# Kernel tuning notes

Measured on AMD Instinct MI355X. Metric: run time of the kernel, lower is better.

## Reference

```python
import jax, jax.numpy as jnp
import numpy as np

B, N, D_NODE, D_PAIR, D_HID = 1, 384, 256, 128, 32
EPS = 1e-5


def setup_inputs() -> dict:
    key = jax.random.key(0)
    ks = jax.random.split(key, 9)
    sc = lambda fan_in: 1.0 / np.sqrt(fan_in)
    return {
        "s": jax.random.normal(ks[0], (B, N, D_NODE), dtype=jnp.float32),
        "gamma": jnp.ones((D_NODE,), dtype=jnp.float32),
        "beta": jnp.zeros((D_NODE,), dtype=jnp.float32),
        "Wa": jax.random.uniform(ks[1], (D_HID, D_NODE), jnp.float32, -sc(D_NODE), sc(D_NODE)),
        "ba": jax.random.uniform(ks[2], (D_HID,), jnp.float32, -sc(D_NODE), sc(D_NODE)),
        "Wb": jax.random.uniform(ks[3], (D_HID, D_NODE), jnp.float32, -sc(D_NODE), sc(D_NODE)),
        "bb": jax.random.uniform(ks[4], (D_HID,), jnp.float32, -sc(D_NODE), sc(D_NODE)),
        "Wo": jax.random.uniform(ks[5], (D_PAIR, D_HID * D_HID), jnp.float32, -sc(D_HID * D_HID), sc(D_HID * D_HID)),
        "bo": jax.random.uniform(ks[6], (D_PAIR,), jnp.float32, -sc(D_HID * D_HID), sc(D_HID * D_HID)),
    }


def reference(s, gamma, beta, Wa, ba, Wb, bb, Wo, bo):
    # LayerNorm over d_node
    mu = jnp.mean(s, axis=-1, keepdims=True)
    var = jnp.mean(jnp.square(s - mu), axis=-1, keepdims=True)
    sn = (s - mu) * jax.lax.rsqrt(var + EPS) * gamma + beta
    # Projections to d_hidden
    a = jnp.einsum('bnd,hd->bnh', sn, Wa) + ba  # [B,N,H]
    b = jnp.einsum('bnd,hd->bnh', sn, Wb) + bb  # [B,N,H]
    # outer[b,i,j,d,e] = a[b,i,d]*b[b,j,e]; reshape flattens (d,e) with d major,
    # matching Wo.reshape(d_pair, H, H). Fuse the outer product with the output
    # projection to avoid materializing the [B,N,N,H,H] tensor.
    Wr = Wo.reshape(D_PAIR, D_HID, D_HID)
    out = jnp.einsum('bid,bje,pde->bijp', a, b, Wr) + bo  # [B,N,N,d_pair]
    return out
```

## Files before the change

### kernel.cpp

```cpp
#include <hip/hip_runtime.h>
#include <hip/hip_bf16.h>

#define NTOK   384
#define DNODE  256
#define DPAIR  128
#define DHID   32
#define NOUT   49152
static constexpr float LN_EPS = 1e-5f;

typedef __bf16 bf16x8 __attribute__((ext_vector_type(8)));
typedef float  f32x4  __attribute__((ext_vector_type(4)));

__global__ __launch_bounds__(256) void k1_ln_proj(
    const float* __restrict__ s, const float* __restrict__ gamma,
    const float* __restrict__ beta,
    const float* __restrict__ Wa, const float* __restrict__ ba,
    const float* __restrict__ Wb, const float* __restrict__ bb,
    const float* __restrict__ Wo,
    __bf16* __restrict__ a_vec, __bf16* __restrict__ b_vec,
    __bf16* __restrict__ wo_bf)
{
    const int t = threadIdx.x;
    const int blk = blockIdx.x;

    if (blk >= NTOK) {
        const int base = (blk - NTOK) * 1024 + t;
        #pragma unroll
        for (int i = 0; i < 4; ++i)
            wo_bf[base + i * 256] = (__bf16)Wo[base + i * 256];
        return;
    }

    __shared__ __align__(16) float sn[DNODE];
    __shared__ float red[8];

    const float x = s[blk * DNODE + t];
    float v0 = x, v1 = x * x;
    #pragma unroll
    for (int off = 32; off > 0; off >>= 1) {
        v0 += __shfl_down(v0, off, 64);
        v1 += __shfl_down(v1, off, 64);
    }
    if ((t & 63) == 0) { red[(t >> 6) * 2] = v0; red[(t >> 6) * 2 + 1] = v1; }
    __syncthreads();
    const float sum   = red[0] + red[2] + red[4] + red[6];
    const float sumsq = red[1] + red[3] + red[5] + red[7];
    const float mu  = sum * (1.0f / DNODE);
    const float var = sumsq * (1.0f / DNODE) - mu * mu;
    const float inv = rsqrtf(var + LN_EPS);
    sn[t] = (x - mu) * inv * gamma[t] + beta[t];
    __syncthreads();

    const int o = t >> 2, part = t & 3;
    const float* Wrow = (o < DHID) ? (Wa + (size_t)o * DNODE)
                                   : (Wb + (size_t)(o - DHID) * DNODE);
    const int base = part * 64;
    float acc = 0.f;
    #pragma unroll
    for (int k = 0; k < 64; k += 4) {
        const float4 w  = *(const float4*)(Wrow + base + k);
        const float4 xs = *(const float4*)(sn + base + k);
        acc += w.x * xs.x + w.y * xs.y + w.z * xs.z + w.w * xs.w;
    }
    acc += __shfl_xor(acc, 1, 64);
    acc += __shfl_xor(acc, 2, 64);
    if (part == 0) {
        if (o < DHID) a_vec[blk * DHID + o]          = (__bf16)(acc + ba[o]);
        else          b_vec[blk * DHID + (o - DHID)] = (__bf16)(acc + bb[o - DHID]);
    }
}

__global__ __launch_bounds__(256) void k2_build_T(
    const __bf16* __restrict__ b_vec, const __bf16* __restrict__ wo_bf,
    __bf16* __restrict__ Tm)
{
    const int l = threadIdx.x & 63;
    const int w = threadIdx.x >> 6;
    const int j0 = blockIdx.y * 16;
    const int n0 = (blockIdx.x * 4 + w) * 16;
    const int row = l & 15, q = l >> 4, koff = q * 8;

    const bf16x8 af = *(const bf16x8*)(b_vec + (j0 + row) * DHID + koff);
    const bf16x8 bf = *(const bf16x8*)(wo_bf + (size_t)(n0 + row) * 32 + koff);
    f32x4 acc = {0.f, 0.f, 0.f, 0.f};
    acc = __builtin_amdgcn_mfma_f32_16x16x32_bf16(af, bf, acc, 0, 0, 0);

    const int col = n0 + row;
    #pragma unroll
    for (int r = 0; r < 4; ++r)
        Tm[(size_t)(j0 + q * 4 + r) * 4096 + col] = (__bf16)acc[r];
}

__global__ __launch_bounds__(256) void k3_main(
    const __bf16* __restrict__ a_vec, const __bf16* __restrict__ Tm,
    const float* __restrict__ bo, float* __restrict__ out)
{
    const int l = threadIdx.x & 63;
    const int w = threadIdx.x >> 6;
    const int i0 = blockIdx.y * 16;
    const int row = l & 15, q = l >> 4, koff = q * 8;

    const bf16x8 af = *(const bf16x8*)(a_vec + (i0 + row) * DHID + koff);

    const int ntb = blockIdx.x * 16 + w * 4;
    #pragma unroll
    for (int tt = 0; tt < 4; ++tt) {
        const int n0 = (ntb + tt) * 16;
        const bf16x8 bf = *(const bf16x8*)(Tm + (size_t)(n0 + row) * 32 + koff);
        const float bv = bo[(n0 + row) & (DPAIR - 1)];
        f32x4 acc = {bv, bv, bv, bv};
        acc = __builtin_amdgcn_mfma_f32_16x16x32_bf16(af, bf, acc, 0, 0, 0);

        const size_t colbase = (size_t)n0 + row;
        #pragma unroll
        for (int r = 0; r < 4; ++r)
            __builtin_nontemporal_store(
                acc[r], out + (size_t)(i0 + q * 4 + r) * NOUT + colbase);
    }
}

extern "C" void kernel_launch(void* const* d_in, const int* in_sizes, int n_in,
                              void* d_out, int out_size, void* d_ws, size_t ws_size,
                              hipStream_t stream)
{
    const float* s     = (const float*)d_in[0];
    const float* gamma = (const float*)d_in[1];
    const float* beta  = (const float*)d_in[2];
    const float* Wa    = (const float*)d_in[3];
    const float* ba    = (const float*)d_in[4];
    const float* Wb    = (const float*)d_in[5];
    const float* bb    = (const float*)d_in[6];
    const float* Wo    = (const float*)d_in[7];
    const float* bo    = (const float*)d_in[8];
    float* out = (float*)d_out;

    char* ws = (char*)d_ws;
    __bf16* a_vec = (__bf16*)(ws);
    __bf16* b_vec = (__bf16*)(ws + 24576);
    __bf16* wo_bf = (__bf16*)(ws + 49152);
    __bf16* Tm    = (__bf16*)(ws + 311296);

    k1_ln_proj<<<512, 256, 0, stream>>>(s, gamma, beta, Wa, ba, Wb, bb, Wo,
                                        a_vec, b_vec, wo_bf);
    k2_build_T<<<dim3(64, 24), 256, 0, stream>>>(b_vec, wo_bf, Tm);
    k3_main<<<dim3(192, 24), 256, 0, stream>>>(a_vec, Tm, bo, out);
}
```

Baseline: 116.6 us.

## Swap MFMA operand roles for vectorized stores and fold Wo bf16 cast into T build

Drops the separate Wo-to-bf16 conversion pass and instead converts Wo inline inside k2, where it is now the A operand. Both k2 and k3 swap MFMA operand roles so each lane holds four consecutive output columns. This lets them use vectorized bf16x4 and float4 nontemporal stores in place of scattered scalar stores. k3 also handles eight tiles per wave with fewer blocks, and the bias is loaded as a float4. The aim is better store coalescing on the large output write and less launch and workspace traffic, at the cost of redoing the fp32-to-bf16 Wo conversion for every j block.

```diff
diff --git a/kernel.cpp b/kernel.cpp
--- a/kernel.cpp
+++ b/kernel.cpp
@@ -9,6 +9,7 @@
 static constexpr float LN_EPS = 1e-5f;
 
 typedef __bf16 bf16x8 __attribute__((ext_vector_type(8)));
+typedef __bf16 bf16x4 __attribute__((ext_vector_type(4)));
 typedef float  f32x4  __attribute__((ext_vector_type(4)));
 
 __global__ __launch_bounds__(256) void k1_ln_proj(
@@ -16,20 +17,10 @@
     const float* __restrict__ beta,
     const float* __restrict__ Wa, const float* __restrict__ ba,
     const float* __restrict__ Wb, const float* __restrict__ bb,
-    const float* __restrict__ Wo,
-    __bf16* __restrict__ a_vec, __bf16* __restrict__ b_vec,
-    __bf16* __restrict__ wo_bf)
+    __bf16* __restrict__ a_vec, __bf16* __restrict__ b_vec)
 {
     const int t = threadIdx.x;
     const int blk = blockIdx.x;
-
-    if (blk >= NTOK) {
-        const int base = (blk - NTOK) * 1024 + t;
-        #pragma unroll
-        for (int i = 0; i < 4; ++i)
-            wo_bf[base + i * 256] = (__bf16)Wo[base + i * 256];
-        return;
-    }
 
     __shared__ __align__(16) float sn[DNODE];
     __shared__ float red[8];
@@ -71,24 +62,37 @@
 }
 
 __global__ __launch_bounds__(256) void k2_build_T(
-    const __bf16* __restrict__ b_vec, const __bf16* __restrict__ wo_bf,
+    const __bf16* __restrict__ b_vec, const float* __restrict__ Wo,
     __bf16* __restrict__ Tm)
 {
     const int l = threadIdx.x & 63;
     const int w = threadIdx.x >> 6;
     const int j0 = blockIdx.y * 16;
-    const int n0 = (blockIdx.x * 4 + w) * 16;
+    const int mg = blockIdx.x * 4 + w;
     const int row = l & 15, q = l >> 4, koff = q * 8;
 
-    const bf16x8 af = *(const bf16x8*)(b_vec + (j0 + row) * DHID + koff);
-    const bf16x8 bf = *(const bf16x8*)(wo_bf + (size_t)(n0 + row) * 32 + koff);
-    f32x4 acc = {0.f, 0.f, 0.f, 0.f};
-    acc = __builtin_amdgcn_mfma_f32_16x16x32_bf16(af, bf, acc, 0, 0, 0);
+    const bf16x8 bfr = *(const bf16x8*)(b_vec + (j0 + row) * DHID + koff);
 
-    const int col = n0 + row;
     #pragma unroll
-    for (int r = 0; r < 4; ++r)
-        Tm[(size_t)(j0 + q * 4 + r) * 4096 + col] = (__bf16)acc[r];
+    for (int tt = 0; tt < 4; ++tt) {
+        const int m0 = (mg * 4 + tt) * 16;
+        const float* wr = Wo + (size_t)(m0 + row) * 32 + koff;
+        const float4 w0 = *(const float4*)(wr);
+        const float4 w1 = *(const float4*)(wr + 4);
+        bf16x8 afr;
+        afr[0] = (__bf16)w0.x; afr[1] = (__bf16)w0.y;
+        afr[2] = (__bf16)w0.z; afr[3] = (__bf16)w0.w;
+        afr[4] = (__bf16)w1.x; afr[5] = (__bf16)w1.y;
+        afr[6] = (__bf16)w1.z; afr[7] = (__bf16)w1.w;
+
+        f32x4 acc = {0.f, 0.f, 0.f, 0.f};
+        acc = __builtin_amdgcn_mfma_f32_16x16x32_bf16(afr, bfr, acc, 0, 0, 0);
+
+        bf16x4 o;
+        o[0] = (__bf16)acc[0]; o[1] = (__bf16)acc[1];
+        o[2] = (__bf16)acc[2]; o[3] = (__bf16)acc[3];
+        *(bf16x4*)(Tm + (size_t)(j0 + row) * 4096 + m0 + q * 4) = o;
+    }
 }
 
 __global__ __launch_bounds__(256) void k3_main(
@@ -100,22 +104,19 @@
     const int i0 = blockIdx.y * 16;
     const int row = l & 15, q = l >> 4, koff = q * 8;
 
-    const bf16x8 af = *(const bf16x8*)(a_vec + (i0 + row) * DHID + koff);
+    const bf16x8 bfr = *(const bf16x8*)(a_vec + (i0 + row) * DHID + koff);
 
-    const int ntb = blockIdx.x * 16 + w * 4;
+    const int g = blockIdx.x * 4 + w;
     #pragma unroll
-    for (int tt = 0; tt < 4; ++tt) {
-        const int n0 = (ntb + tt) * 16;
-        const bf16x8 bf = *(const bf16x8*)(Tm + (size_t)(n0 + row) * 32 + koff);
-        const float bv = bo[(n0 + row) & (DPAIR - 1)];
-        f32x4 acc = {bv, bv, bv, bv};
-        acc = __builtin_amdgcn_mfma_f32_16x16x32_bf16(af, bf, acc, 0, 0, 0);
+    for (int tt = 0; tt < 8; ++tt) {
+        const int jp0 = (g * 8 + tt) * 16;
+        const bf16x8 afr = *(const bf16x8*)(Tm + (size_t)(jp0 + row) * 32 + koff);
+        const float4 bv = *(const float4*)(bo + ((jp0 & (DPAIR - 1)) + q * 4));
+        f32x4 acc = {bv.x, bv.y, bv.z, bv.w};
+        acc = __builtin_amdgcn_mfma_f32_16x16x32_bf16(afr, bfr, acc, 0, 0, 0);
 
-        const size_t colbase = (size_t)n0 + row;
-        #pragma unroll
-        for (int r = 0; r < 4; ++r)
-            __builtin_nontemporal_store(
-                acc[r], out + (size_t)(i0 + q * 4 + r) * NOUT + colbase);
+        f32x4* dst = (f32x4*)(out + (size_t)(i0 + row) * NOUT + jp0 + q * 4);
+        __builtin_nontemporal_store(acc, dst);
     }
 }
 
@@ -137,11 +138,10 @@
     char* ws = (char*)d_ws;
     __bf16* a_vec = (__bf16*)(ws);
     __bf16* b_vec = (__bf16*)(ws + 24576);
-    __bf16* wo_bf = (__bf16*)(ws + 49152);
-    __bf16* Tm    = (__bf16*)(ws + 311296);
+    __bf16* Tm    = (__bf16*)(ws + 49152);
 
-    k1_ln_proj<<<512, 256, 0, stream>>>(s, gamma, beta, Wa, ba, Wb, bb, Wo,
-                                        a_vec, b_vec, wo_bf);
-    k2_build_T<<<dim3(64, 24), 256, 0, stream>>>(b_vec, wo_bf, Tm);
-    k3_main<<<dim3(192, 24), 256, 0, stream>>>(a_vec, Tm, bo, out);
+    k1_ln_proj<<<384, 256, 0, stream>>>(s, gamma, beta, Wa, ba, Wb, bb,
+                                        a_vec, b_vec);
+    k2_build_T<<<dim3(16, 24), 256, 0, stream>>>(b_vec, Wo, Tm);
+    k3_main<<<dim3(96, 24), 256, 0, stream>>>(a_vec, Tm, bo, out);
 }
```

After: 116.5 us. Within noise of the previous version (-0.1%).
